# Kernel optimization log

Hardware: AMD Instinct MI355X
Metric: run time of the kernel (lower is better)

## Reference

```python
import jax, jax.numpy as jnp
import numpy as np

N = 8192
IN_F = 512
OUT_F = 64
ALPHA = 0.2  # LeakyReLU negative slope
NEG_INF = -9e15


def setup_inputs() -> dict:
    key = jax.random.key(0)
    k1, k2, k3, k4 = jax.random.split(key, 4)
    inp = jax.random.normal(k1, (N, IN_F), dtype=jnp.float32)
    adj = jax.random.randint(k2, (N, N), 0, 2, dtype=jnp.int32)
    W = jax.random.normal(k3, (IN_F, OUT_F), dtype=jnp.float32) * (1.414 * (6.0 / (IN_F + OUT_F)) ** 0.5)
    a = jax.random.normal(k4, (2 * OUT_F, 1), dtype=jnp.float32) * (1.414 * (6.0 / (2 * OUT_F + 1)) ** 0.5)
    return {"input": inp, "adj": adj, "W": W, "a": a}


def reference(input, adj, W, a):
    h = input @ W                      # [N, F]
    F_ = h.shape[1]
    # e_ij = leakyrelu(a[:F].h_i + a[F:].h_j)  (equivalent to the concat form)
    f_src = h @ a[:F_, 0]              # [N]
    f_dst = h @ a[F_:, 0]              # [N]
    e = jax.nn.leaky_relu(f_src[:, None] + f_dst[None, :], negative_slope=ALPHA)  # [N, N]
    att = jnp.where(adj > 0, e, jnp.float32(NEG_INF))
    att = jax.nn.softmax(att, axis=1)  # dropout p is inert in eval mode
    h_prime = att @ h                  # [N, F]
    return jax.nn.elu(h_prime)         # concat=True
```

## Files before the change

### kernel.cpp

```cpp
#include <hip/hip_runtime.h>

#define N_NODES 8192
#define IN_F 512
#define OUT_F 64
#define LOG2E 1.4426950408889634f

typedef short bf16x8 __attribute__((ext_vector_type(8)));
typedef float f32x4 __attribute__((ext_vector_type(4)));

static __device__ __forceinline__ unsigned short f2bf(float f) {
  unsigned u = __float_as_uint(f);
  u = (u + 0x7fffu + ((u >> 16) & 1u)) >> 16;
  return (unsigned short)u;
}

__global__ __launch_bounds__(256) void k_gemm(const float* __restrict__ input,
                                              const float* __restrict__ W,
                                              const float* __restrict__ a,
                                              float* __restrict__ h,
                                              float* __restrict__ fsrcL,
                                              float* __restrict__ fdstL) {
  const int lane = threadIdx.x & 63;
  const int wv = threadIdx.x >> 6;
  const int row = blockIdx.x * 4 + wv;
  const float* inrow = input + (size_t)row * IN_F;
  const int c = lane;
  float acc = 0.f;
  for (int k = 0; k < IN_F; k += 4) {
    float4 x = *(const float4*)(inrow + k);
    acc += x.x * W[(k + 0) * OUT_F + c];
    acc += x.y * W[(k + 1) * OUT_F + c];
    acc += x.z * W[(k + 2) * OUT_F + c];
    acc += x.w * W[(k + 3) * OUT_F + c];
  }
  h[(size_t)row * OUT_F + c] = acc;
  float vs = acc * a[c];
  float vd = acc * a[OUT_F + c];
#pragma unroll
  for (int off = 32; off > 0; off >>= 1) {
    vs += __shfl_xor(vs, off, 64);
    vd += __shfl_xor(vd, off, 64);
  }
  if (lane == 0) {
    fsrcL[row] = vs * LOG2E;
    fdstL[row] = vd * LOG2E;
  }
}

__global__ __launch_bounds__(256) void k_max(const float* __restrict__ fdstL,
                                             float* __restrict__ ML) {
  float m = -3.0e38f;
  for (int i = threadIdx.x; i < N_NODES; i += 256) m = fmaxf(m, fdstL[i]);
#pragma unroll
  for (int off = 32; off > 0; off >>= 1) m = fmaxf(m, __shfl_xor(m, off, 64));
  __shared__ float sm[4];
  if ((threadIdx.x & 63) == 0) sm[threadIdx.x >> 6] = m;
  __syncthreads();
  if (threadIdx.x == 0) ML[0] = fmaxf(fmaxf(sm[0], sm[1]), fmaxf(sm[2], sm[3]));
}

__global__ __launch_bounds__(256) void k_transpose(const float* __restrict__ h,
                                                   unsigned short* __restrict__ hT) {
  __shared__ float t[64][65];
  const int r0 = blockIdx.x * 64;
#pragma unroll
  for (int q = 0; q < 16; q++) {
    int idx = q * 256 + threadIdx.x;
    int r = idx >> 6, c = idx & 63;
    t[c][r] = h[(size_t)(r0 + r) * OUT_F + c];
  }
  __syncthreads();
#pragma unroll
  for (int q = 0; q < 8; q++) {
    int idx = q * 256 + threadIdx.x;
    int c = idx >> 5, rp = idx & 31;
    float a0 = t[c][2 * rp], a1 = t[c][2 * rp + 1];
    unsigned pk = (unsigned)f2bf(a0) | ((unsigned)f2bf(a1) << 16);
    *(unsigned*)(hT + (size_t)c * N_NODES + r0 + 2 * rp) = pk;
  }
}

__global__ __launch_bounds__(256) void k_attn(const int* __restrict__ adj,
                                              const unsigned short* __restrict__ hT,
                                              const float* __restrict__ fsrcL,
                                              const float* __restrict__ fdstL,
                                              const float* __restrict__ MLp,
                                              float* __restrict__ out) {
  const int lane = threadIdx.x & 63;
  const int wv = threadIdx.x >> 6;
  const int i0 = blockIdx.x * 16;
  const int m = lane & 15;
  const int g = lane >> 4;

  const float MLv = MLp[0];
  const float fs = fsrcL[i0 + m];
  const float xm = fs + MLv;
  const float mL = fmaxf(xm, 0.2f * xm);

  f32x4 acc0{}, acc1{}, acc2{}, acc3{};
  float lpart = 0.f;

  const int* adjrow = adj + (size_t)(i0 + m) * N_NODES;
  const unsigned short* hT0 = hT + (size_t)m * N_NODES;

  const int jbeg = wv * (N_NODES / 4);
  const int jend = jbeg + (N_NODES / 4);
  for (int j0 = jbeg; j0 < jend; j0 += 64) {
#pragma unroll
    for (int s = 0; s < 2; s++) {
      const int jb = j0 + s * 32 + g * 8;
      int4 a0 = *(const int4*)(adjrow + jb);
      int4 a1 = *(const int4*)(adjrow + jb + 4);
      float4 d0 = *(const float4*)(fdstL + jb);
      float4 d1 = *(const float4*)(fdstL + jb + 4);
      bf16x8 b0 = *(const bf16x8*)(hT0 + jb);
      bf16x8 b1 = *(const bf16x8*)(hT0 + (size_t)16 * N_NODES + jb);
      bf16x8 b2 = *(const bf16x8*)(hT0 + (size_t)32 * N_NODES + jb);
      bf16x8 b3 = *(const bf16x8*)(hT0 + (size_t)48 * N_NODES + jb);

      int av[8] = {a0.x, a0.y, a0.z, a0.w, a1.x, a1.y, a1.z, a1.w};
      float dv[8] = {d0.x, d0.y, d0.z, d0.w, d1.x, d1.y, d1.z, d1.w};
      bf16x8 pa;
#pragma unroll
      for (int t = 0; t < 8; t++) {
        float x = fs + dv[t];
        float y = fmaxf(x, 0.2f * x) - mL;
        float p = __builtin_amdgcn_exp2f(y);
        p = av[t] ? p : 0.0f;
        lpart += p;
        pa[t] = (short)f2bf(p);
      }
      acc0 = __builtin_amdgcn_mfma_f32_16x16x32_bf16(pa, b0, acc0, 0, 0, 0);
      acc1 = __builtin_amdgcn_mfma_f32_16x16x32_bf16(pa, b1, acc1, 0, 0, 0);
      acc2 = __builtin_amdgcn_mfma_f32_16x16x32_bf16(pa, b2, acc2, 0, 0, 0);
      acc3 = __builtin_amdgcn_mfma_f32_16x16x32_bf16(pa, b3, acc3, 0, 0, 0);
    }
  }

  lpart += __shfl_xor(lpart, 16, 64);
  lpart += __shfl_xor(lpart, 32, 64);

  __shared__ float accbuf[4][16][64];
  __shared__ float lbuf[4][16];
#pragma unroll
  for (int r = 0; r < 4; r++) {
    accbuf[wv][g * 4 + r][0 + m]  = acc0[r];
    accbuf[wv][g * 4 + r][16 + m] = acc1[r];
    accbuf[wv][g * 4 + r][32 + m] = acc2[r];
    accbuf[wv][g * 4 + r][48 + m] = acc3[r];
  }
  if (lane < 16) lbuf[wv][lane] = lpart;
  __syncthreads();

#pragma unroll
  for (int q = 0; q < 4; q++) {
    int idx = q * 256 + threadIdx.x;
    int r = idx >> 6, c = idx & 63;
    float ssum = accbuf[0][r][c] + accbuf[1][r][c] + accbuf[2][r][c] + accbuf[3][r][c];
    float l = lbuf[0][r] + lbuf[1][r] + lbuf[2][r] + lbuf[3][r];
    float v = ssum / l;
    out[(size_t)(i0 + r) * OUT_F + c] =
        v > 0.f ? v : __builtin_amdgcn_exp2f(v * LOG2E) - 1.f;
  }
}

extern "C" void kernel_launch(void* const* d_in, const int* in_sizes, int n_in,
                              void* d_out, int out_size, void* d_ws, size_t ws_size,
                              hipStream_t stream) {
  const float* input = (const float*)d_in[0];
  const int* adj = (const int*)d_in[1];
  const float* W = (const float*)d_in[2];
  const float* a = (const float*)d_in[3];
  float* out = (float*)d_out;

  char* ws = (char*)d_ws;
  float* h = (float*)ws;
  unsigned short* hT = (unsigned short*)(ws + (2u << 20));
  float* fsrcL = (float*)(ws + (3u << 20));
  float* fdstL = (float*)(ws + (3u << 20) + 32 * 1024);
  float* ML = (float*)(ws + (3u << 20) + 64 * 1024);

  k_gemm<<<N_NODES / 4, 256, 0, stream>>>(input, W, a, h, fsrcL, fdstL);
  k_max<<<1, 256, 0, stream>>>(fdstL, ML);
  k_transpose<<<N_NODES / 64, 256, 0, stream>>>(h, hT);
  k_attn<<<N_NODES / 16, 256, 0, stream>>>(adj, hT, fsrcL, fdstL, ML, out);
}
```

Before: 480.2 us.

## Pack adjacency into bitmask in a pre-pass and widen attention blocks to 8 waves

Adds a kernel that converts the int32 adjacency matrix into a 1-bit-per-edge mask. The attention kernel then reads 64-bit mask words instead of int32 entries. The attention block grows from 4 to 8 waves, each covering a shorter stretch of columns, with a larger shared-memory reduction at the end. The full adjacency still has to be read once in the pack pass, so the main saving is decoupling that stream from the compute-heavy kernel, at the cost of an extra launch and mask writes.

```diff
diff --git a/kernel.cpp b/kernel.cpp
--- a/kernel.cpp
+++ b/kernel.cpp
@@ -12,6 +12,27 @@
   unsigned u = __float_as_uint(f);
   u = (u + 0x7fffu + ((u >> 16) & 1u)) >> 16;
   return (unsigned short)u;
+}
+
+__global__ __launch_bounds__(256) void k_pack(const int* __restrict__ adj,
+                                              unsigned* __restrict__ mask) {
+  __shared__ unsigned char nib[256];
+  const int tid = threadIdx.x;
+  for (int it = 0; it < 16; ++it) {
+    int g4 = blockIdx.x * (256 * 16) + it * 256 + tid;
+    int4 v = ((const int4*)adj)[g4];
+    unsigned n = (unsigned)(v.x != 0) | ((unsigned)(v.y != 0) << 1) |
+                 ((unsigned)(v.z != 0) << 2) | ((unsigned)(v.w != 0) << 3);
+    __syncthreads();
+    nib[tid] = (unsigned char)n;
+    __syncthreads();
+    if (tid < 32) {
+      unsigned w = 0;
+#pragma unroll
+      for (int i = 0; i < 8; ++i) w |= ((unsigned)nib[tid * 8 + i]) << (4 * i);
+      mask[blockIdx.x * 512 + it * 32 + tid] = w;
+    }
+  }
 }
 
 __global__ __launch_bounds__(256) void k_gemm(const float* __restrict__ input,
@@ -80,7 +101,7 @@
   }
 }
 
-__global__ __launch_bounds__(256) void k_attn(const int* __restrict__ adj,
+__global__ __launch_bounds__(512) void k_attn(const unsigned long long* __restrict__ mask,
                                               const unsigned short* __restrict__ hT,
                                               const float* __restrict__ fsrcL,
                                               const float* __restrict__ fdstL,
@@ -100,17 +121,16 @@
   f32x4 acc0{}, acc1{}, acc2{}, acc3{};
   float lpart = 0.f;
 
-  const int* adjrow = adj + (size_t)(i0 + m) * N_NODES;
+  const unsigned long long* mrow = mask + (size_t)(i0 + m) * (N_NODES / 64);
   const unsigned short* hT0 = hT + (size_t)m * N_NODES;
 
-  const int jbeg = wv * (N_NODES / 4);
-  const int jend = jbeg + (N_NODES / 4);
+  const int jbeg = wv * (N_NODES / 8);
+  const int jend = jbeg + (N_NODES / 8);
   for (int j0 = jbeg; j0 < jend; j0 += 64) {
+    unsigned long long M = mrow[j0 >> 6];
 #pragma unroll
     for (int s = 0; s < 2; s++) {
       const int jb = j0 + s * 32 + g * 8;
-      int4 a0 = *(const int4*)(adjrow + jb);
-      int4 a1 = *(const int4*)(adjrow + jb + 4);
       float4 d0 = *(const float4*)(fdstL + jb);
       float4 d1 = *(const float4*)(fdstL + jb + 4);
       bf16x8 b0 = *(const bf16x8*)(hT0 + jb);
@@ -118,7 +138,7 @@
       bf16x8 b2 = *(const bf16x8*)(hT0 + (size_t)32 * N_NODES + jb);
       bf16x8 b3 = *(const bf16x8*)(hT0 + (size_t)48 * N_NODES + jb);
 
-      int av[8] = {a0.x, a0.y, a0.z, a0.w, a1.x, a1.y, a1.z, a1.w};
+      unsigned mb = (unsigned)(M >> (s * 32 + g * 8)) & 0xffu;
       float dv[8] = {d0.x, d0.y, d0.z, d0.w, d1.x, d1.y, d1.z, d1.w};
       bf16x8 pa;
 #pragma unroll
@@ -126,7 +146,7 @@
         float x = fs + dv[t];
         float y = fmaxf(x, 0.2f * x) - mL;
         float p = __builtin_amdgcn_exp2f(y);
-        p = av[t] ? p : 0.0f;
+        p = (mb >> t) & 1u ? p : 0.0f;
         lpart += p;
         pa[t] = (short)f2bf(p);
       }
@@ -140,11 +160,11 @@
   lpart += __shfl_xor(lpart, 16, 64);
   lpart += __shfl_xor(lpart, 32, 64);
 
-  __shared__ float accbuf[4][16][64];
-  __shared__ float lbuf[4][16];
+  __shared__ float accbuf[8][16][64];
+  __shared__ float lbuf[8][16];
 #pragma unroll
   for (int r = 0; r < 4; r++) {
-    accbuf[wv][g * 4 + r][0 + m]  = acc0[r];
+    accbuf[wv][g * 4 + r][0 + m] = acc0[r];
     accbuf[wv][g * 4 + r][16 + m] = acc1[r];
     accbuf[wv][g * 4 + r][32 + m] = acc2[r];
     accbuf[wv][g * 4 + r][48 + m] = acc3[r];
@@ -153,11 +173,15 @@
   __syncthreads();
 
 #pragma unroll
-  for (int q = 0; q < 4; q++) {
-    int idx = q * 256 + threadIdx.x;
+  for (int q = 0; q < 2; q++) {
+    int idx = q * 512 + threadIdx.x;
     int r = idx >> 6, c = idx & 63;
-    float ssum = accbuf[0][r][c] + accbuf[1][r][c] + accbuf[2][r][c] + accbuf[3][r][c];
-    float l = lbuf[0][r] + lbuf[1][r] + lbuf[2][r] + lbuf[3][r];
+    float ssum = 0.f, l = 0.f;
+#pragma unroll
+    for (int w = 0; w < 8; w++) {
+      ssum += accbuf[w][r][c];
+      l += lbuf[w][r];
+    }
     float v = ssum / l;
     out[(size_t)(i0 + r) * OUT_F + c] =
         v > 0.f ? v : __builtin_amdgcn_exp2f(v * LOG2E) - 1.f;
@@ -179,9 +203,12 @@
   float* fsrcL = (float*)(ws + (3u << 20));
   float* fdstL = (float*)(ws + (3u << 20) + 32 * 1024);
   float* ML = (float*)(ws + (3u << 20) + 64 * 1024);
-
+  unsigned* mask = (unsigned*)(ws + (4u << 20));
+
+  k_pack<<<4096, 256, 0, stream>>>(adj, mask);
   k_gemm<<<N_NODES / 4, 256, 0, stream>>>(input, W, a, h, fsrcL, fdstL);
   k_max<<<1, 256, 0, stream>>>(fdstL, ML);
   k_transpose<<<N_NODES / 64, 256, 0, stream>>>(h, hT);
-  k_attn<<<N_NODES / 16, 256, 0, stream>>>(adj, hT, fsrcL, fdstL, ML, out);
-}
+  k_attn<<<N_NODES / 16, 512, 0, stream>>>((const unsigned long long*)mask, hT,
+                                           fsrcL, fdstL, ML, out);
+}
```

Measured after the change: 525.2 us. 9.4% more time.
